# Optimization experiments

Measured on AMD Instinct MI355X. Metric: run time of the kernel, lower is better.

## Reference

```python
import jax, jax.numpy as jnp
import numpy as np

N_NODES = 50000
N_EDGES = 800000
N_GRAPHS = 256
F_IN = 256
H_DIM = 64


def setup_inputs() -> dict:
    key = jax.random.key(0)
    ks = jax.random.split(key, 9)
    x = jax.random.normal(ks[0], (N_NODES, F_IN), dtype=jnp.float32)
    edge_index = jax.random.randint(ks[1], (2, N_EDGES), 0, N_NODES, dtype=jnp.int64)
    batch = jnp.sort(jax.random.randint(ks[2], (N_NODES,), 0, N_GRAPHS, dtype=jnp.int64))
    s = 1.0 / np.sqrt(F_IN)
    Wq = jax.random.normal(ks[3], (F_IN, H_DIM), dtype=jnp.float32) * s
    bq = jnp.zeros((H_DIM,), dtype=jnp.float32)
    Wk = jax.random.normal(ks[4], (F_IN, H_DIM), dtype=jnp.float32) * s
    bk = jnp.zeros((H_DIM,), dtype=jnp.float32)
    Wv = jax.random.normal(ks[5], (F_IN, H_DIM), dtype=jnp.float32) * s
    bv = jnp.zeros((H_DIM,), dtype=jnp.float32)
    return {"x": x, "Wq": Wq, "bq": bq, "Wk": Wk, "bk": bk, "Wv": Wv, "bv": bv,
            "edge_index": edge_index, "batch": batch}


def reference(x, Wq, bq, Wk, bk, Wv, bv, edge_index, batch):
    src, dest = edge_index[0], edge_index[1]
    # node projections then per-edge gathers
    q = (x @ Wq + bq)[dest]            # [E, h]
    k = (x @ Wk + bk)[src]             # [E, h]
    v = (x @ Wv + bv)[src]             # [E, h]
    # per-edge dot-product score (bmm of [E,1,h] x [E,h,1])
    prod = jnp.sum(k * q, axis=-1, keepdims=True) / np.sqrt(H_DIM)  # [E, 1]
    exp = jnp.exp(prod)
    seg = batch[src]                   # per-graph segment of source node
    denom = jax.ops.segment_sum(exp, seg, num_segments=N_GRAPHS)    # [G, 1]
    a = exp / (denom[seg] + 1e-6)      # [E, 1]
    out = jax.ops.segment_sum(v * a, dest, num_segments=N_NODES)    # [N, h]
    return out
```

## Files before the change

kernel.cpp:

```cpp
#include <hip/hip_runtime.h>

#define H    64
#define F    256
#define NSEG 256
#define SCB  2048
#define MB   64
#define KC   64
#define NSPAN_MAX 8192

typedef float          f32x4v __attribute__((ext_vector_type(4)));
typedef short          bf16x8 __attribute__((ext_vector_type(8)));
typedef unsigned short u16x4  __attribute__((ext_vector_type(4)));

__global__ __launch_bounds__(1024) void hist8_kernel(
    const int* __restrict__ ei, int* __restrict__ counts8,
    int N, int E, int nspan)
{
    __shared__ int lh[NSPAN_MAX];
    const int p  = blockIdx.x & 7;
    const int c  = blockIdx.x >> 3;
    const int lo = p * nspan;
    const int span = min(N - lo, nspan);
    const int t = threadIdx.x;

    for (int i = t; i < span; i += 1024) lh[i] = 0;
    __syncthreads();

    const int epc = (E + 7) >> 3;
    const int e0 = c * epc;
    const int e1 = min(E, e0 + epc);

    if (((E + e0) & 3) == 0) {
        const int nv = (e1 - e0) >> 2;
        for (int i = t; i < nv; i += 1024) {
            const int4 d4 = *(const int4*)(ei + E + e0 + i * 4);
            int d;
            d = min(max(d4.x, 0), N - 1) - lo; if ((unsigned)d < (unsigned)span) atomicAdd(&lh[d], 1);
            d = min(max(d4.y, 0), N - 1) - lo; if ((unsigned)d < (unsigned)span) atomicAdd(&lh[d], 1);
            d = min(max(d4.z, 0), N - 1) - lo; if ((unsigned)d < (unsigned)span) atomicAdd(&lh[d], 1);
            d = min(max(d4.w, 0), N - 1) - lo; if ((unsigned)d < (unsigned)span) atomicAdd(&lh[d], 1);
        }
        for (int e = e0 + nv * 4 + t; e < e1; e += 1024) {
            const int d = min(max(ei[E + e], 0), N - 1) - lo;
            if ((unsigned)d < (unsigned)span) atomicAdd(&lh[d], 1);
        }
    } else {
        for (int e = e0 + t; e < e1; e += 1024) {
            const int d = min(max(ei[E + e], 0), N - 1) - lo;
            if ((unsigned)d < (unsigned)span) atomicAdd(&lh[d], 1);
        }
    }
    __syncthreads();

    for (int i = t; i < span; i += 1024) counts8[(size_t)c * N + lo + i] = lh[i];
}

#define CVT_WRITE(buf, rr, cc, val) do {                                      \
    const float ff_[4] = {(val).x, (val).y, (val).z, (val).w};                \
    u16x4 h_, l_;                                                             \
    _Pragma("unroll")                                                         \
    for (int u_ = 0; u_ < 4; ++u_) {                                          \
        unsigned ub_ = __float_as_uint(ff_[u_]);                              \
        h_[u_] = (unsigned short)(ub_ >> 16);                                 \
        float rf_ = ff_[u_] - __uint_as_float(ub_ & 0xFFFF0000u);             \
        l_[u_] = (unsigned short)(__float_as_uint(rf_) >> 16);                \
    }                                                                         \
    const int so_ = (rr) * 64 + (((((cc) >> 1) ^ ((rr) & 7))) << 3)           \
                  + ((cc) & 1) * 4;                                           \
    *(u16x4*)&xs_hi[buf][so_] = h_;                                           \
    *(u16x4*)&xs_lo[buf][so_] = l_;                                           \
} while (0)

__global__ __launch_bounds__(768, 3) void qkv_mfma(
    const float* __restrict__ x,
    const float* __restrict__ Wq, const float* __restrict__ Wk,
    const float* __restrict__ Wv,
    const float* __restrict__ bq, const float* __restrict__ bk,
    const float* __restrict__ bv,
    float* __restrict__ q, float* __restrict__ k, float* __restrict__ v,
    int N, int ntiles)
{
    __shared__ unsigned short xs_hi[2][MB * 64];
    __shared__ unsigned short xs_lo[2][MB * 64];

    const int t    = threadIdx.x;
    const int lane = t & 63;
    const int w    = t >> 6;
    const int mat  = w >> 2;
    const int ct   = w & 3;
    const int l15  = lane & 15;
    const int quad = lane >> 4;

    const float* Wm   = (mat == 0) ? Wq : (mat == 1) ? Wk : Wv;
    const float* bias = (mat == 0) ? bq : (mat == 1) ? bk : bv;
    float*       dst  = (mat == 0) ? q  : (mat == 1) ? k  : v;
    const int col = ct * 16 + l15;
    const float bb = bias[col];

    bf16x8 Bh[8], Bl[8];
    #pragma unroll
    for (int u = 0; u < 8; ++u) {
        #pragma unroll
        for (int j = 0; j < 8; ++j) {
            const float f = Wm[(size_t)(u * 32 + quad * 8 + j) * H + col];
            const unsigned ub = __float_as_uint(f);
            Bh[u][j] = (short)(ub >> 16);
            const float rf = f - __uint_as_float(ub & 0xFFFF0000u);
            Bl[u][j] = (short)(__float_as_uint(rf) >> 16);
        }
    }

    const int r0 = t >> 4;
    const int c0 = t & 15;
    const int r1 = (t + 768) >> 4;

    const int swz = (l15 & 7);

    #pragma unroll 1
    for (int tile = blockIdx.x; tile < ntiles; tile += gridDim.x) {
        const int block0 = tile * MB;

        f32x4v acc[4];
        #pragma unroll
        for (int i = 0; i < 4; ++i) acc[i] = (f32x4v)0.f;

        float4 pv0, pv1;
        pv0 = *(const float4*)(x + (size_t)min(block0 + r0, N - 1) * F + c0 * 4);
        if (t < 256)
            pv1 = *(const float4*)(x + (size_t)min(block0 + r1, N - 1) * F + c0 * 4);
        CVT_WRITE(0, r0, c0, pv0);
        if (t < 256) CVT_WRITE(0, r1, c0, pv1);

        #pragma unroll
        for (int c = 0; c < 4; ++c) {
            __syncthreads();

            if (c < 3) {
                const int kb = (c + 1) * KC;
                pv0 = *(const float4*)(x + (size_t)min(block0 + r0, N - 1) * F + kb + c0 * 4);
                if (t < 256)
                    pv1 = *(const float4*)(x + (size_t)min(block0 + r1, N - 1) * F + kb + c0 * 4);
            }

            #pragma unroll
            for (int sk = 0; sk < 2; ++sk) {
                const int u = c * 2 + sk;
                #pragma unroll
                for (int mt = 0; mt < 4; ++mt) {
                    const int row = mt * 16 + l15;
                    const int ao  = row * 64 + (((sk * 4 + quad) ^ swz) << 3);
                    const bf16x8 ah = *(const bf16x8*)&xs_hi[c & 1][ao];
                    const bf16x8 al = *(const bf16x8*)&xs_lo[c & 1][ao];
                    f32x4v a = acc[mt];
                    a = __builtin_amdgcn_mfma_f32_16x16x32_bf16(ah, Bh[u], a, 0, 0, 0);
                    a = __builtin_amdgcn_mfma_f32_16x16x32_bf16(ah, Bl[u], a, 0, 0, 0);
                    a = __builtin_amdgcn_mfma_f32_16x16x32_bf16(al, Bh[u], a, 0, 0, 0);
                    acc[mt] = a;
                }
            }

            if (c < 3) {
                const int nb = (c & 1) ^ 1;
                CVT_WRITE(nb, r0, c0, pv0);
                if (t < 256) CVT_WRITE(nb, r1, c0, pv1);
            }
        }

        #pragma unroll
        for (int mt = 0; mt < 4; ++mt) {
            #pragma unroll
            for (int r = 0; r < 4; ++r) {
                const int node = block0 + mt * 16 + quad * 4 + r;
                if (node < N)
                    dst[(size_t)node * H + col] = acc[mt][r] + bb;
            }
        }
    }
}

__global__ __launch_bounds__(256) void scanA(
    const int* __restrict__ counts8, int* __restrict__ counts,
    int* __restrict__ offsets, int* __restrict__ bsum, int n)
{
    __shared__ int ps[256];
    const int t = threadIdx.x;
    const int i0 = blockIdx.x * SCB + t * 8;
    int loc[8];
    int s = 0;
    #pragma unroll
    for (int u = 0; u < 8; ++u) {
        int i = i0 + u;
        int c = 0;
        if (i < n) {
            #pragma unroll
            for (int p = 0; p < 8; ++p) c += counts8[(size_t)p * n + i];
            counts[i] = c;
            c = (c + 3) & ~3;
        }
        loc[u] = s; s += c;
    }
    ps[t] = s;
    __syncthreads();
    for (int off = 1; off < 256; off <<= 1) {
        int a = (t >= off) ? ps[t - off] : 0;
        __syncthreads();
        ps[t] += a;
        __syncthreads();
    }
    const int base = ps[t] - s;
    #pragma unroll
    for (int u = 0; u < 8; ++u) {
        int i = i0 + u;
        if (i < n) offsets[i] = base + loc[u];
    }
    if (t == 255) bsum[blockIdx.x] = ps[255];
}

__global__ void scanB(int* __restrict__ bsum, int nb)
{
    const int t = threadIdx.x;
    int v = (t < nb) ? bsum[t] : 0;
    int inc = v;
    #pragma unroll
    for (int off = 1; off < 64; off <<= 1) {
        int u = __shfl_up(inc, off, 64);
        if (t >= off) inc += u;
    }
    if (t < nb) bsum[t] = inc - v;
}

__global__ __launch_bounds__(256) void scanC(
    const int* __restrict__ bsum, int* __restrict__ offsets,
    int* __restrict__ cursor, int n)
{
    const int i0 = blockIdx.x * SCB + threadIdx.x * 8;
    const int add = bsum[blockIdx.x];
    #pragma unroll
    for (int u = 0; u < 8; ++u) {
        int i = i0 + u;
        if (i < n) { int o = offsets[i] + add; offsets[i] = o; cursor[i] = o; }
    }
}

__global__ __launch_bounds__(256) void reorder_kernel(
    const int* __restrict__ ei, const int* __restrict__ batch,
    int* __restrict__ cursor, unsigned* __restrict__ epack,
    int E, int N, int nspan)
{
    const int p  = blockIdx.x & 7;
    const int ci = blockIdx.x >> 3;
    const int lo = p * nspan;
    const int hi = min(N, lo + nspan);
    const int e0 = ci * 1024 + threadIdx.x * 4;

    int d[4];
    if (e0 + 3 < E) {
        const int4 d4 = *(const int4*)(ei + E + e0);
        d[0] = d4.x; d[1] = d4.y; d[2] = d4.z; d[3] = d4.w;
    } else {
        #pragma unroll
        for (int u = 0; u < 4; ++u)
            d[u] = (e0 + u < E) ? ei[E + e0 + u] : -1;
    }

    #pragma unroll
    for (int u = 0; u < 4; ++u) {
        const int dst = min(max(d[u], 0), N - 1);
        if (d[u] >= 0 && dst >= lo && dst < hi) {
            int src = ei[e0 + u];
            src = min(max(src, 0), N - 1);
            int seg = batch[src];
            seg = min(max(seg, 0), NSEG - 1);
            const int pos = atomicAdd(&cursor[dst], 1);
            epack[pos] = (unsigned)src | ((unsigned)seg << 16);
        }
    }
}

__global__ __launch_bounds__(256) void score_kernel(
    const float* __restrict__ q, const float* __restrict__ k,
    const unsigned* __restrict__ epack,
    const int* __restrict__ offsets, const int* __restrict__ counts,
    float* __restrict__ exps, float* __restrict__ denom8, int N)
{
    __shared__ float sden[NSEG];
    const int t = threadIdx.x;
    sden[t] = 0.f;
    __syncthreads();

    const int lane16 = t & 15;
    const int grp    = (t >> 4) & 3;
    const int wave   = t >> 6;
    const int nwaves = gridDim.x * 4;

    const float4* q4 = (const float4*)q;
    const float4* k4 = (const float4*)k;

    for (int n = blockIdx.x * 4 + wave; n < N; n += nwaves) {
        const int off = offsets[n];
        const int cnt = counts[n];
        if (cnt == 0) continue;
        const float4 qv = q4[(size_t)n * 16 + lane16];
        for (int i0 = grp * 4; i0 < cnt; i0 += 16) {
            const uint4 pp = *(const uint4*)(epack + off + i0);
            const unsigned pk[4] = {pp.x, pp.y, pp.z, pp.w};
            const int rem = cnt - i0;
            float4 kv[4];
            #pragma unroll
            for (int u = 0; u < 4; ++u) {
                const int src = min((int)(pk[u] & 0xFFFF), N - 1);
                kv[u] = k4[(size_t)src * 16 + lane16];
            }
            float d[4];
            #pragma unroll
            for (int u = 0; u < 4; ++u) {
                float dd = kv[u].x * qv.x + kv[u].y * qv.y
                         + kv[u].z * qv.z + kv[u].w * qv.w;
                dd += __shfl_xor(dd, 1, 64);
                dd += __shfl_xor(dd, 2, 64);
                dd += __shfl_xor(dd, 4, 64);
                dd += __shfl_xor(dd, 8, 64);
                d[u] = dd;
            }
            if (lane16 == 0) {
                #pragma unroll
                for (int u = 0; u < 4; ++u) {
                    if (u < rem) {
                        const float ex = __expf(d[u] * 0.125f);
                        exps[off + i0 + u] = ex;
                        atomicAdd(&sden[(pk[u] >> 16) & 255], ex);
                    }
                }
            }
        }
    }
    __syncthreads();
    float ds = sden[t];
    if (ds != 0.f) atomicAdd(&denom8[(blockIdx.x & 7) * NSEG + t], ds);
}

__global__ __launch_bounds__(256) void accum_kernel(
    const float* __restrict__ v, const float* __restrict__ exps,
    const unsigned* __restrict__ epack,
    const int* __restrict__ offsets, const int* __restrict__ counts,
    const float* __restrict__ denom8, float* __restrict__ out, int N)
{
    __shared__ float rden[NSEG];
    const int t = threadIdx.x;
    {
        float dsum = 0.f;
        #pragma unroll
        for (int p = 0; p < 8; ++p) dsum += denom8[p * NSEG + t];
        rden[t] = 1.0f / (dsum + 1e-6f);
    }
    __syncthreads();

    const int lane = t & 63;
    const int wave = t >> 6;
    const int n = blockIdx.x * 4 + wave;
    if (n >= N) return;

    const int off = offsets[n];
    const int cnt = counts[n];

    float acc = 0.f;
    int i = 0;
    for (; i + 8 <= cnt; i += 8) {
        const uint4  pa = *(const uint4*)(epack + off + i);
        const uint4  pb = *(const uint4*)(epack + off + i + 4);
        const float4 ea = *(const float4*)(exps + off + i);
        const float4 eb = *(const float4*)(exps + off + i + 4);
        const float v0 = v[(size_t)(pa.x & 0xFFFF) * H + lane];
        const float v1 = v[(size_t)(pa.y & 0xFFFF) * H + lane];
        const float v2 = v[(size_t)(pa.z & 0xFFFF) * H + lane];
        const float v3 = v[(size_t)(pa.w & 0xFFFF) * H + lane];
        const float v4_ = v[(size_t)(pb.x & 0xFFFF) * H + lane];
        const float v5 = v[(size_t)(pb.y & 0xFFFF) * H + lane];
        const float v6 = v[(size_t)(pb.z & 0xFFFF) * H + lane];
        const float v7 = v[(size_t)(pb.w & 0xFFFF) * H + lane];
        acc = fmaf(v0, ea.x * rden[(pa.x >> 16) & 255], acc);
        acc = fmaf(v1, ea.y * rden[(pa.y >> 16) & 255], acc);
        acc = fmaf(v2, ea.z * rden[(pa.z >> 16) & 255], acc);
        acc = fmaf(v3, ea.w * rden[(pa.w >> 16) & 255], acc);
        acc = fmaf(v4_, eb.x * rden[(pb.x >> 16) & 255], acc);
        acc = fmaf(v5, eb.y * rden[(pb.y >> 16) & 255], acc);
        acc = fmaf(v6, eb.z * rden[(pb.z >> 16) & 255], acc);
        acc = fmaf(v7, eb.w * rden[(pb.w >> 16) & 255], acc);
    }
    for (; i + 4 <= cnt; i += 4) {
        const uint4  pp = *(const uint4*)(epack + off + i);
        const float4 ee = *(const float4*)(exps + off + i);
        const float v0 = v[(size_t)(pp.x & 0xFFFF) * H + lane];
        const float v1 = v[(size_t)(pp.y & 0xFFFF) * H + lane];
        const float v2 = v[(size_t)(pp.z & 0xFFFF) * H + lane];
        const float v3 = v[(size_t)(pp.w & 0xFFFF) * H + lane];
        acc = fmaf(v0, ee.x * rden[(pp.x >> 16) & 255], acc);
        acc = fmaf(v1, ee.y * rden[(pp.y >> 16) & 255], acc);
        acc = fmaf(v2, ee.z * rden[(pp.z >> 16) & 255], acc);
        acc = fmaf(v3, ee.w * rden[(pp.w >> 16) & 255], acc);
    }
    for (; i < cnt; ++i) {
        const unsigned p = epack[off + i];
        acc = fmaf(v[(size_t)(p & 0xFFFF) * H + lane],
                   exps[off + i] * rden[(p >> 16) & 255], acc);
    }
    out[(size_t)n * H + lane] = acc;
}

extern "C" void kernel_launch(void* const* d_in, const int* in_sizes, int n_in,
                              void* d_out, int out_size, void* d_ws, size_t ws_size,
                              hipStream_t stream)
{
    const float* x   = (const float*)d_in[0];
    const float* Wq  = (const float*)d_in[1];
    const float* bq  = (const float*)d_in[2];
    const float* Wk  = (const float*)d_in[3];
    const float* bk  = (const float*)d_in[4];
    const float* Wv  = (const float*)d_in[5];
    const float* bv  = (const float*)d_in[6];
    const int* ei    = (const int*)d_in[7];
    const int* batch = (const int*)d_in[8];

    const int N = in_sizes[8];
    const int E = in_sizes[7] / 2;
    const int EP = E + 3 * N + 16;

    float*    q       = (float*)d_ws;
    float*    k       = q + (size_t)N * H;
    float*    v       = k + (size_t)N * H;
    float*    exps    = v + (size_t)N * H;
    unsigned* epack   = (unsigned*)(exps + EP);
    int*      counts  = (int*)(epack + EP);
    int*      offsets = counts + N;
    int*      cursor  = offsets + N;
    int*      bsum    = cursor + N;
    float*    denom8  = (float*)(bsum + 64);
    int*      counts8 = (int*)(denom8 + 8 * NSEG);

    hipMemsetAsync(denom8, 0, 8 * NSEG * sizeof(float), stream);

    const int NT    = (N + MB - 1) / MB;
    const int NC    = (E + 1023) / 1024;
    const int nspan = (N + 7) / 8;
    const int NBSC  = (N + SCB - 1) / SCB;

    hist8_kernel<<<64, 1024, 0, stream>>>(ei, counts8, N, E, nspan);

    qkv_mfma<<<256, 768, 0, stream>>>(
        x, Wq, Wk, Wv, bq, bk, bv, q, k, v, N, NT);

    scanA<<<NBSC, 256, 0, stream>>>(counts8, counts, offsets, bsum, N);
    scanB<<<1, 64, 0, stream>>>(bsum, NBSC);
    scanC<<<NBSC, 256, 0, stream>>>(bsum, offsets, cursor, N);

    reorder_kernel<<<8 * NC, 256, 0, stream>>>(
        ei, batch, cursor, epack, E, N, nspan);

    score_kernel<<<2048, 256, 0, stream>>>(
        q, k, epack, offsets, counts, exps, denom8, N);

    accum_kernel<<<(N + 3) / 4, 256, 0, stream>>>(
        v, exps, epack, offsets, counts, denom8, (float*)d_out, N);
}
```

Before: 260.1 us.

## Use per-chunk LDS cursors in reorder to avoid global atomics

The CSR build now splits edges into 16 chunks instead of 8. scanC computes a separate starting cursor for each (chunk, node span) pair. The reorder kernel loads those cursors into shared memory and uses LDS atomics in place of global atomicAdd on one cursor per node. This removes contended global atomics in the scatter, at the cost of extra countsC/cursorC traffic and fewer, larger reorder blocks (128 blocks of 1024 threads) that each scan a full edge chunk.

```diff
diff --git a/kernel.cpp b/kernel.cpp
--- a/kernel.cpp
+++ b/kernel.cpp
@@ -7,13 +7,14 @@
 #define MB   64
 #define KC   64
 #define NSPAN_MAX 8192
+#define NCHUNK 16
 
 typedef float          f32x4v __attribute__((ext_vector_type(4)));
 typedef short          bf16x8 __attribute__((ext_vector_type(8)));
 typedef unsigned short u16x4  __attribute__((ext_vector_type(4)));
 
-__global__ __launch_bounds__(1024) void hist8_kernel(
-    const int* __restrict__ ei, int* __restrict__ counts8,
+__global__ __launch_bounds__(1024) void hist_kernel(
+    const int* __restrict__ ei, int* __restrict__ countsC,
     int N, int E, int nspan)
 {
     __shared__ int lh[NSPAN_MAX];
@@ -26,11 +27,11 @@
     for (int i = t; i < span; i += 1024) lh[i] = 0;
     __syncthreads();
 
-    const int epc = (E + 7) >> 3;
+    const int epc = (E + NCHUNK - 1) / NCHUNK;
     const int e0 = c * epc;
     const int e1 = min(E, e0 + epc);
 
-    if (((E + e0) & 3) == 0) {
+    if (((E | e0) & 3) == 0) {
         const int nv = (e1 - e0) >> 2;
         for (int i = t; i < nv; i += 1024) {
             const int4 d4 = *(const int4*)(ei + E + e0 + i * 4);
@@ -52,7 +53,7 @@
     }
     __syncthreads();
 
-    for (int i = t; i < span; i += 1024) counts8[(size_t)c * N + lo + i] = lh[i];
+    for (int i = t; i < span; i += 1024) countsC[(size_t)c * N + lo + i] = lh[i];
 }
 
 #define CVT_WRITE(buf, rr, cc, val) do {                                      \
@@ -179,7 +180,7 @@
 }
 
 __global__ __launch_bounds__(256) void scanA(
-    const int* __restrict__ counts8, int* __restrict__ counts,
+    const int* __restrict__ countsC, int* __restrict__ counts,
     int* __restrict__ offsets, int* __restrict__ bsum, int n)
 {
     __shared__ int ps[256];
@@ -193,7 +194,7 @@
         int c = 0;
         if (i < n) {
             #pragma unroll
-            for (int p = 0; p < 8; ++p) c += counts8[(size_t)p * n + i];
+            for (int p = 0; p < NCHUNK; ++p) c += countsC[(size_t)p * n + i];
             counts[i] = c;
             c = (c + 3) & ~3;
         }
@@ -230,49 +231,80 @@
 }
 
 __global__ __launch_bounds__(256) void scanC(
-    const int* __restrict__ bsum, int* __restrict__ offsets,
-    int* __restrict__ cursor, int n)
+    const int* __restrict__ bsum, const int* __restrict__ countsC,
+    int* __restrict__ offsets, int* __restrict__ cursorC, int n)
 {
     const int i0 = blockIdx.x * SCB + threadIdx.x * 8;
     const int add = bsum[blockIdx.x];
     #pragma unroll
     for (int u = 0; u < 8; ++u) {
         int i = i0 + u;
-        if (i < n) { int o = offsets[i] + add; offsets[i] = o; cursor[i] = o; }
-    }
-}
-
-__global__ __launch_bounds__(256) void reorder_kernel(
+        if (i < n) {
+            int o = offsets[i] + add;
+            offsets[i] = o;
+            #pragma unroll
+            for (int p = 0; p < NCHUNK; ++p) {
+                cursorC[(size_t)p * n + i] = o;
+                o += countsC[(size_t)p * n + i];
+            }
+        }
+    }
+}
+
+__global__ __launch_bounds__(1024) void reorder_kernel(
     const int* __restrict__ ei, const int* __restrict__ batch,
-    int* __restrict__ cursor, unsigned* __restrict__ epack,
+    const int* __restrict__ cursorC, unsigned* __restrict__ epack,
     int E, int N, int nspan)
 {
+    __shared__ int lcur[NSPAN_MAX];
     const int p  = blockIdx.x & 7;
-    const int ci = blockIdx.x >> 3;
+    const int c  = blockIdx.x >> 3;
     const int lo = p * nspan;
-    const int hi = min(N, lo + nspan);
-    const int e0 = ci * 1024 + threadIdx.x * 4;
-
-    int d[4];
-    if (e0 + 3 < E) {
-        const int4 d4 = *(const int4*)(ei + E + e0);
-        d[0] = d4.x; d[1] = d4.y; d[2] = d4.z; d[3] = d4.w;
+    const int span = min(N - lo, nspan);
+    const int t = threadIdx.x;
+
+    for (int i = t; i < span; i += 1024) lcur[i] = cursorC[(size_t)c * N + lo + i];
+    __syncthreads();
+
+    const int epc = (E + NCHUNK - 1) / NCHUNK;
+    const int e0 = c * epc;
+    const int e1 = min(E, e0 + epc);
+
+    if (((E | e0) & 3) == 0) {
+        const int nv = (e1 - e0) >> 2;
+        for (int i = t; i < nv; i += 1024) {
+            const int eb = e0 + i * 4;
+            const int4 d4 = *(const int4*)(ei + E + eb);
+            const int dd[4] = {d4.x, d4.y, d4.z, d4.w};
+            #pragma unroll
+            for (int u = 0; u < 4; ++u) {
+                const int d = min(max(dd[u], 0), N - 1) - lo;
+                if ((unsigned)d < (unsigned)span) {
+                    const int pos = atomicAdd(&lcur[d], 1);
+                    const int src = min(max(ei[eb + u], 0), N - 1);
+                    const int seg = min(max(batch[src], 0), NSEG - 1);
+                    epack[pos] = (unsigned)src | ((unsigned)seg << 16);
+                }
+            }
+        }
+        for (int e = e0 + nv * 4 + t; e < e1; e += 1024) {
+            const int d = min(max(ei[E + e], 0), N - 1) - lo;
+            if ((unsigned)d < (unsigned)span) {
+                const int pos = atomicAdd(&lcur[d], 1);
+                const int src = min(max(ei[e], 0), N - 1);
+                const int seg = min(max(batch[src], 0), NSEG - 1);
+                epack[pos] = (unsigned)src | ((unsigned)seg << 16);
+            }
+        }
     } else {
-        #pragma unroll
-        for (int u = 0; u < 4; ++u)
-            d[u] = (e0 + u < E) ? ei[E + e0 + u] : -1;
-    }
-
-    #pragma unroll
-    for (int u = 0; u < 4; ++u) {
-        const int dst = min(max(d[u], 0), N - 1);
-        if (d[u] >= 0 && dst >= lo && dst < hi) {
-            int src = ei[e0 + u];
-            src = min(max(src, 0), N - 1);
-            int seg = batch[src];
-            seg = min(max(seg, 0), NSEG - 1);
-            const int pos = atomicAdd(&cursor[dst], 1);
-            epack[pos] = (unsigned)src | ((unsigned)seg << 16);
+        for (int e = e0 + t; e < e1; e += 1024) {
+            const int d = min(max(ei[E + e], 0), N - 1) - lo;
+            if ((unsigned)d < (unsigned)span) {
+                const int pos = atomicAdd(&lcur[d], 1);
+                const int src = min(max(ei[e], 0), N - 1);
+                const int seg = min(max(batch[src], 0), NSEG - 1);
+                epack[pos] = (unsigned)src | ((unsigned)seg << 16);
+            }
         }
     }
 }
@@ -432,29 +464,28 @@
     unsigned* epack   = (unsigned*)(exps + EP);
     int*      counts  = (int*)(epack + EP);
     int*      offsets = counts + N;
-    int*      cursor  = offsets + N;
-    int*      bsum    = cursor + N;
+    int*      bsum    = offsets + N;
     float*    denom8  = (float*)(bsum + 64);
-    int*      counts8 = (int*)(denom8 + 8 * NSEG);
+    int*      countsC = (int*)(denom8 + 8 * NSEG);
+    int*      cursorC = countsC + (size_t)NCHUNK * N;
 
     hipMemsetAsync(denom8, 0, 8 * NSEG * sizeof(float), stream);
 
     const int NT    = (N + MB - 1) / MB;
-    const int NC    = (E + 1023) / 1024;
     const int nspan = (N + 7) / 8;
     const int NBSC  = (N + SCB - 1) / SCB;
 
-    hist8_kernel<<<64, 1024, 0, stream>>>(ei, counts8, N, E, nspan);
+    hist_kernel<<<8 * NCHUNK, 1024, 0, stream>>>(ei, countsC, N, E, nspan);
 
     qkv_mfma<<<256, 768, 0, stream>>>(
         x, Wq, Wk, Wv, bq, bk, bv, q, k, v, N, NT);
 
-    scanA<<<NBSC, 256, 0, stream>>>(counts8, counts, offsets, bsum, N);
+    scanA<<<NBSC, 256, 0, stream>>>(countsC, counts, offsets, bsum, N);
     scanB<<<1, 64, 0, stream>>>(bsum, NBSC);
-    scanC<<<NBSC, 256, 0, stream>>>(bsum, offsets, cursor, N);
-
-    reorder_kernel<<<8 * NC, 256, 0, stream>>>(
-        ei, batch, cursor, epack, E, N, nspan);
+    scanC<<<NBSC, 256, 0, stream>>>(bsum, countsC, offsets, cursorC, N);
+
+    reorder_kernel<<<8 * NCHUNK, 1024, 0, stream>>>(
+        ei, batch, cursorC, epack, E, N, nspan);
 
     score_kernel<<<2048, 256, 0, stream>>>(
         q, k, epack, offsets, counts, exps, denom8, N);
```

After: 279.6 us. 1.07x slower.
